# Optimization experiments

Hardware: AMD Instinct MI355X
Metric: run time of the kernel (lower is better)

Reference implementation:

```python
import jax, jax.numpy as jnp
import numpy as np
from jax import lax

B, T, I, H = 32, 512, 512, 1024


def setup_inputs() -> dict:
    key = jax.random.key(0)
    k0, k1, k2, k3, k4 = jax.random.split(key, 5)
    s_i = 1.0 / np.sqrt(I).astype(np.float32)
    s_h = 1.0 / np.sqrt(H).astype(np.float32)
    x = jax.random.normal(k0, (B, T, I), dtype=jnp.float32)
    # stacked gate weights, order: input(i), forget(f), cell(g), output(o)
    Wx = jax.random.uniform(k1, (4 * H, I), jnp.float32, -s_i, s_i)
    bx = jax.random.uniform(k2, (4 * H,), jnp.float32, -s_i, s_i)
    Wh = jax.random.uniform(k3, (4 * H, H), jnp.float32, -s_h, s_h)
    bh = jax.random.uniform(k4, (4 * H,), jnp.float32, -s_h, s_h)
    return {"x": x, "Wx": Wx, "bx": bx, "Wh": Wh, "bh": bh}


def reference(x, Wx, bx, Wh, bh):
    # Pre-compute all input-to-gate projections in one batched GEMM: [B,T,4H]
    xg = jnp.einsum("bti,gi->btg", x, Wx) + bx + bh

    def step(carry, xg_t):
        h, c = carry
        gates = xg_t + h @ Wh.T  # [B,4H]
        i, f, g, o = jnp.split(gates, 4, axis=-1)
        i = jax.nn.sigmoid(i)
        f = jax.nn.sigmoid(f)
        g = jnp.tanh(g)
        o = jax.nn.sigmoid(o)
        c = f * c + i * g
        h = o * jnp.tanh(c)  # r is None in forward -> h_tilde = tanh(c)
        return (h, c), h

    b = x.shape[0]
    h0 = jnp.zeros((b, H), dtype=x.dtype)
    c0 = jnp.zeros((b, H), dtype=x.dtype)
    _, hs = lax.scan(step, (h0, c0), jnp.swapaxes(xg, 0, 1))  # hs: [T,B,H]
    return jnp.swapaxes(hs, 0, 1)  # [B,T,H]
```

## Files before the change

kernel.cpp:

```cpp
#include <hip/hip_runtime.h>
#include <hip/hip_bf16.h>

#define Bv 32
#define Tv 512
#define Iv 512
#define Hv 1024
#define NG 4096

typedef short bf16x8 __attribute__((ext_vector_type(8)));
typedef float floatx16 __attribute__((ext_vector_type(16)));
typedef unsigned short u16;
typedef unsigned long long u64;

__device__ __forceinline__ u16 f2bf(float f) {
  __hip_bfloat16 h = __float2bfloat16(f);
  return *reinterpret_cast<u16*>(&h);
}

__device__ __forceinline__ floatx16 mfma32(bf16x8 a, bf16x8 b, floatx16 c) {
  return __builtin_amdgcn_mfma_f32_32x32x16_bf16(a, b, c, 0, 0, 0);
}

__device__ __forceinline__ u64 ld_agent_u64(const u64* p) {
  return __hip_atomic_load(p, __ATOMIC_RELAXED, __HIP_MEMORY_SCOPE_AGENT);
}
__device__ __forceinline__ void st_agent_u16(u16* p, u16 v) {
  __hip_atomic_store(p, v, __ATOMIC_RELAXED, __HIP_MEMORY_SCOPE_AGENT);
}

__device__ __forceinline__ bf16x8 mk_frag(u64 lo, u64 hi) {
  union { u64 q[2]; bf16x8 v; } u;
  u.q[0] = lo; u.q[1] = hi;
  return u.v;
}

__global__ void k_init(unsigned int* p, int n) {
  int i = blockIdx.x * blockDim.x + threadIdx.x;
  if (i < n) p[i] = 0u;
}

__global__ void k_f2bf(const float* __restrict__ in, u16* __restrict__ out, int n) {
  int i = blockIdx.x * blockDim.x + threadIdx.x;
  if (i < n) out[i] = f2bf(in[i]);
}

__global__ void k_whf(const float* __restrict__ Wh, u16* __restrict__ whf) {
  int tid = blockIdx.x * 256 + threadIdx.x;
  int lane = tid & 63;
  int kt   = (tid >> 6) & 63;
  int nt   = (tid >> 12) & 1;
  int bl   = tid >> 13;
  int r    = nt * 32 + (lane & 31);
  int gate = r >> 4, du = r & 15;
  int row  = gate * Hv + bl * 16 + du;
  int k0   = kt * 16 + (lane >> 5) * 8;
  const float* s = Wh + (size_t)row * Hv + k0;
  u16* d = whf + (size_t)tid * 8;
#pragma unroll
  for (int j = 0; j < 8; ++j) d[j] = f2bf(s[j]);
}

__global__ __launch_bounds__(256) void k_xg(const u16* __restrict__ xb, const u16* __restrict__ wxb,
                                            const float* __restrict__ bx, const float* __restrict__ bh,
                                            float* __restrict__ xg, int t0, int tcshift) {
  __shared__ u16 Al[128 * 40];
  __shared__ u16 Bl[128 * 40];
  int tid = threadIdx.x;
  int wave = tid >> 6, lane = tid & 63;
  int wm = wave & 1, wn = wave >> 1;
  int bm = blockIdx.x, bn = blockIdx.y;
  int Tc = 1 << tcshift;

  floatx16 acc[2][2];
#pragma unroll
  for (int a = 0; a < 2; ++a)
#pragma unroll
    for (int c = 0; c < 2; ++c)
#pragma unroll
      for (int r = 0; r < 16; ++r) acc[a][c][r] = 0.f;

  int lr = tid >> 1;
  int lk = (tid & 1) * 16;
  int m  = bm * 128 + lr;
  int b  = m >> tcshift;
  int tl = m & (Tc - 1);
  const u16* asrc = xb + (size_t)(b * Tv + t0 + tl) * Iv + lk;
  int nrow = bn * 128 + lr;
  const u16* bsrc = wxb + (size_t)nrow * Iv + lk;
  u16* adst = &Al[lr * 40 + lk];
  u16* bdst = &Bl[lr * 40 + lk];

  for (int k0 = 0; k0 < Iv; k0 += 32) {
    __syncthreads();
    *(uint4*)adst       = *(const uint4*)(asrc);
    *(uint4*)(adst + 8) = *(const uint4*)(asrc + 8);
    *(uint4*)bdst       = *(const uint4*)(bsrc);
    *(uint4*)(bdst + 8) = *(const uint4*)(bsrc + 8);
    asrc += 32; bsrc += 32;
    __syncthreads();
#pragma unroll
    for (int kt = 0; kt < 2; ++kt) {
      int ko = kt * 16 + (lane >> 5) * 8;
      bf16x8 a0 = *(const bf16x8*)(&Al[(wm * 64 +      (lane & 31)) * 40 + ko]);
      bf16x8 a1 = *(const bf16x8*)(&Al[(wm * 64 + 32 + (lane & 31)) * 40 + ko]);
      bf16x8 b0 = *(const bf16x8*)(&Bl[(wn * 64 +      (lane & 31)) * 40 + ko]);
      bf16x8 b1 = *(const bf16x8*)(&Bl[(wn * 64 + 32 + (lane & 31)) * 40 + ko]);
      acc[0][0] = mfma32(a0, b0, acc[0][0]);
      acc[0][1] = mfma32(a0, b1, acc[0][1]);
      acc[1][0] = mfma32(a1, b0, acc[1][0]);
      acc[1][1] = mfma32(a1, b1, acc[1][1]);
    }
  }
#pragma unroll
  for (int mt = 0; mt < 2; ++mt) {
#pragma unroll
    for (int ntt = 0; ntt < 2; ++ntt) {
      int nGl = bn * 128 + wn * 64 + ntt * 32 + (lane & 31);
      float bias = bx[nGl] + bh[nGl];
#pragma unroll
      for (int r = 0; r < 16; ++r) {
        int mrow = (r & 3) + 8 * (r >> 2) + 4 * (lane >> 5);
        int mG = bm * 128 + wm * 64 + mt * 32 + mrow;
        int bb = mG >> tcshift;
        int tt = mG & (Tc - 1);
        xg[((size_t)(tt * Bv + bb) << 12) + nGl] = acc[mt][ntt][r] + bias;
      }
    }
  }
}

__global__ __launch_bounds__(256, 1) void k_scan(const u16* __restrict__ whf, const float* __restrict__ xg,
                                                 u64* __restrict__ hA, float* __restrict__ cbuf,
                                                 float* __restrict__ out, int* cnt, int t0, int Tc) {
  __shared__ float red[4][64][36];
  int tid = threadIdx.x;
  int bl = blockIdx.x;
  int kh = tid >> 6, lane = tid & 63;
  int eu = tid & 15, eb = tid >> 4;
  int u0 = bl * 16;

  bf16x8 w0[16], w1[16];
  {
    const u16* wb0 = whf + ((size_t)(bl * 2 + 0) << 15);
    const u16* wb1 = whf + ((size_t)(bl * 2 + 1) << 15);
#pragma unroll
    for (int kk = 0; kk < 16; ++kk) {
      int kt = kh * 16 + kk;
      w0[kk] = *(const bf16x8*)(wb0 + (size_t)((kt << 6) + lane) * 8);
      w1[kk] = *(const bf16x8*)(wb1 + (size_t)((kt << 6) + lane) * 8);
    }
  }

  float c0, c1;
  if (t0 == 0) { c0 = 0.f; c1 = 0.f; }
  else {
    c0 = cbuf[eb * Hv + u0 + eu];
    c1 = cbuf[(eb + 16) * Hv + u0 + eu];
  }

  u16* hA16 = (u16*)hA;

  float xgv[4][2];
#pragma unroll
  for (int g = 0; g < 4; ++g)
#pragma unroll
    for (int b2 = 0; b2 < 2; ++b2)
      xgv[g][b2] = xg[((size_t)(0 * Bv + eb + 16 * b2) << 12) + g * Hv + u0 + eu];

  for (int tl = 0; tl < Tc; ++tl) {
    int t = t0 + tl;
    const u64* hAr = hA + (size_t)(t & 1) * 8192;

    floatx16 acc0, acc1;
#pragma unroll
    for (int r = 0; r < 16; ++r) { acc0[r] = 0.f; acc1[r] = 0.f; }
#pragma unroll
    for (int kk = 0; kk < 16; ++kk) {
      int kt = kh * 16 + kk;
      size_t fi = (size_t)((kt << 6) + lane) * 2;
      bf16x8 a = mk_frag(ld_agent_u64(hAr + fi), ld_agent_u64(hAr + fi + 1));
      acc0 = mfma32(a, w0[kk], acc0);
      acc1 = mfma32(a, w1[kk], acc1);
    }

    {
      int n = lane & 31;
      int bq = 4 * (lane >> 5);
#pragma unroll
      for (int rq = 0; rq < 4; ++rq) {
        float4 v0 = make_float4(acc0[rq * 4 + 0], acc0[rq * 4 + 1], acc0[rq * 4 + 2], acc0[rq * 4 + 3]);
        float4 v1 = make_float4(acc1[rq * 4 + 0], acc1[rq * 4 + 1], acc1[rq * 4 + 2], acc1[rq * 4 + 3]);
        *(float4*)&red[kh][n][8 * rq + bq]      = v0;
        *(float4*)&red[kh][32 + n][8 * rq + bq] = v1;
      }
    }

    float xgn[4][2];
    {
      int tln = (tl + 1 < Tc) ? tl + 1 : tl;
#pragma unroll
      for (int g = 0; g < 4; ++g)
#pragma unroll
        for (int b2 = 0; b2 < 2; ++b2)
          xgn[g][b2] = xg[((size_t)(tln * Bv + eb + 16 * b2) << 12) + g * Hv + u0 + eu];
    }

    __syncthreads();

    u16* hAw16 = hA16 + (size_t)((t + 1) & 1) * 32768;
#pragma unroll
    for (int b2 = 0; b2 < 2; ++b2) {
      int b = eb + 16 * b2;
      float gsum[4];
#pragma unroll
      for (int g = 0; g < 4; ++g) {
        int r = g * 16 + eu;
        gsum[g] = red[0][r][b] + red[1][r][b] + red[2][r][b] + red[3][r][b] + xgv[g][b2];
      }
      float iv = 1.f / (1.f + __expf(-gsum[0]));
      float fv = 1.f / (1.f + __expf(-gsum[1]));
      float gv = 1.f - 2.f / (__expf(2.f * gsum[2]) + 1.f);
      float ov = 1.f / (1.f + __expf(-gsum[3]));
      float& c = b2 ? c1 : c0;
      c = fv * c + iv * gv;
      float hval = ov * (1.f - 2.f / (__expf(2.f * c) + 1.f));
      st_agent_u16(hAw16 + ((size_t)((bl << 6) + b + ((eu >> 3) << 5)) << 3) + (eu & 7), f2bf(hval));
      out[((size_t)(b * Tv + t) << 10) + u0 + eu] = hval;
    }

    asm volatile("s_waitcnt vmcnt(0)" ::: "memory");
    __syncthreads();
    if (tid == 0) {
      __hip_atomic_fetch_add(cnt, 1, __ATOMIC_RELAXED, __HIP_MEMORY_SCOPE_AGENT);
      int target = 64 * (t + 1);
      while (__hip_atomic_load(cnt, __ATOMIC_RELAXED, __HIP_MEMORY_SCOPE_AGENT) < target) { }
    }
    __syncthreads();

#pragma unroll
    for (int g = 0; g < 4; ++g)
#pragma unroll
      for (int b2 = 0; b2 < 2; ++b2) xgv[g][b2] = xgn[g][b2];
  }
  cbuf[eb * Hv + u0 + eu] = c0;
  cbuf[(eb + 16) * Hv + u0 + eu] = c1;
}

extern "C" void kernel_launch(void* const* d_in, const int* in_sizes, int n_in,
                              void* d_out, int out_size, void* d_ws, size_t ws_size,
                              hipStream_t stream) {
  const float* x  = (const float*)d_in[0];
  const float* Wx = (const float*)d_in[1];
  const float* bx = (const float*)d_in[2];
  const float* Wh = (const float*)d_in[3];
  const float* bh = (const float*)d_in[4];
  float* out = (float*)d_out;
  char* ws = (char*)d_ws;

  int*   cnt = (int*)ws;
  u64*   hA  = (u64*)(ws + 4096);
  float* cb  = (float*)(ws + 4096 + (128 << 10));
  u16*   xb  = (u16*)(ws + 4096 + (256 << 10));
  u16*   wxb = xb + (size_t)Bv * Tv * Iv;
  u16*   whf = wxb + (size_t)NG * Iv;
  float* xg  = (float*)(whf + (size_t)64 * 2 * 64 * 64 * 8);

  size_t fixedB = 4096 + (256ull << 10) +
                  ((size_t)Bv * Tv * Iv + (size_t)NG * Iv + (size_t)64 * 2 * 64 * 64 * 8) * 2;
  int tcshift = 9;
  while (tcshift > 2 && fixedB + (((size_t)Bv * NG * 4) << tcshift) > ws_size) --tcshift;
  int Tc = 1 << tcshift;

  k_init<<<132, 256, 0, stream>>>((unsigned int*)ws, (4096 + (128 << 10)) / 4);
  k_f2bf<<<(Bv * Tv * Iv) / 256, 256, 0, stream>>>(x, xb, Bv * Tv * Iv);
  k_f2bf<<<(NG * Iv) / 256, 256, 0, stream>>>(Wx, wxb, NG * Iv);
  k_whf<<<2048, 256, 0, stream>>>(Wh, whf);

  for (int t0 = 0; t0 < Tv; t0 += Tc) {
    k_xg<<<dim3(Tc / 4, 32), 256, 0, stream>>>(xb, wxb, bx, bh, xg, t0, tcshift);
    k_scan<<<64, 256, 0, stream>>>(whf, xg, hA, cb, out, cnt, t0, Tc);
  }
}
```

Baseline: 2.675 ms.

## Replace atomic counter barrier with per-block flags and batch h loads

Replaces the single contended atomic-add counter grid barrier with per-block step flags: each block stores its step number and one wavefront polls all 64 flags, combining them with a wave vote. All h-fragment loads are now issued up front, before the MFMA chain, so their latency overlaps, and the Wh fragments are pinned in AGPRs with asm constraints. The reduction scratch is padded to 33 columns and written with scalar stores instead of float4. The aim is lower per-step barrier and load latency in the sequential scan, at the cost of more polling traffic and registers.

```diff
diff --git a/kernel.cpp b/kernel.cpp
--- a/kernel.cpp
+++ b/kernel.cpp
@@ -131,8 +131,8 @@
 
 __global__ __launch_bounds__(256, 1) void k_scan(const u16* __restrict__ whf, const float* __restrict__ xg,
                                                  u64* __restrict__ hA, float* __restrict__ cbuf,
-                                                 float* __restrict__ out, int* cnt, int t0, int Tc) {
-  __shared__ float red[4][64][36];
+                                                 float* __restrict__ out, int* flg, int t0, int Tc) {
+  __shared__ float red[4][64][33];
   int tid = threadIdx.x;
   int bl = blockIdx.x;
   int kh = tid >> 6, lane = tid & 63;
@@ -148,6 +148,8 @@
       int kt = kh * 16 + kk;
       w0[kk] = *(const bf16x8*)(wb0 + (size_t)((kt << 6) + lane) * 8);
       w1[kk] = *(const bf16x8*)(wb1 + (size_t)((kt << 6) + lane) * 8);
+      asm("" : "+a"(w0[kk]));
+      asm("" : "+a"(w1[kk]));
     }
   }
 
@@ -171,30 +173,13 @@
     int t = t0 + tl;
     const u64* hAr = hA + (size_t)(t & 1) * 8192;
 
-    floatx16 acc0, acc1;
-#pragma unroll
-    for (int r = 0; r < 16; ++r) { acc0[r] = 0.f; acc1[r] = 0.f; }
+    u64 alo[16], ahi[16];
 #pragma unroll
     for (int kk = 0; kk < 16; ++kk) {
-      int kt = kh * 16 + kk;
-      size_t fi = (size_t)((kt << 6) + lane) * 2;
-      bf16x8 a = mk_frag(ld_agent_u64(hAr + fi), ld_agent_u64(hAr + fi + 1));
-      acc0 = mfma32(a, w0[kk], acc0);
-      acc1 = mfma32(a, w1[kk], acc1);
-    }
-
-    {
-      int n = lane & 31;
-      int bq = 4 * (lane >> 5);
-#pragma unroll
-      for (int rq = 0; rq < 4; ++rq) {
-        float4 v0 = make_float4(acc0[rq * 4 + 0], acc0[rq * 4 + 1], acc0[rq * 4 + 2], acc0[rq * 4 + 3]);
-        float4 v1 = make_float4(acc1[rq * 4 + 0], acc1[rq * 4 + 1], acc1[rq * 4 + 2], acc1[rq * 4 + 3]);
-        *(float4*)&red[kh][n][8 * rq + bq]      = v0;
-        *(float4*)&red[kh][32 + n][8 * rq + bq] = v1;
-      }
-    }
-
+      size_t fi = (size_t)(((kh * 16 + kk) << 6) + lane) * 2;
+      alo[kk] = ld_agent_u64(hAr + fi);
+      ahi[kk] = ld_agent_u64(hAr + fi + 1);
+    }
     float xgn[4][2];
     {
       int tln = (tl + 1 < Tc) ? tl + 1 : tl;
@@ -205,6 +190,26 @@
           xgn[g][b2] = xg[((size_t)(tln * Bv + eb + 16 * b2) << 12) + g * Hv + u0 + eu];
     }
 
+    floatx16 acc0, acc1;
+#pragma unroll
+    for (int r = 0; r < 16; ++r) { acc0[r] = 0.f; acc1[r] = 0.f; }
+#pragma unroll
+    for (int kk = 0; kk < 16; ++kk) {
+      bf16x8 a = mk_frag(alo[kk], ahi[kk]);
+      acc0 = mfma32(a, w0[kk], acc0);
+      acc1 = mfma32(a, w1[kk], acc1);
+    }
+
+    {
+      int n = lane & 31;
+      int hoff = 4 * (lane >> 5);
+#pragma unroll
+      for (int r = 0; r < 16; ++r) {
+        int b = (r & 3) + 8 * (r >> 2) + hoff;
+        red[kh][n][b]      = acc0[r];
+        red[kh][32 + n][b] = acc1[r];
+      }
+    }
     __syncthreads();
 
     u16* hAw16 = hA16 + (size_t)((t + 1) & 1) * 32768;
@@ -230,10 +235,14 @@
 
     asm volatile("s_waitcnt vmcnt(0)" ::: "memory");
     __syncthreads();
-    if (tid == 0) {
-      __hip_atomic_fetch_add(cnt, 1, __ATOMIC_RELAXED, __HIP_MEMORY_SCOPE_AGENT);
-      int target = 64 * (t + 1);
-      while (__hip_atomic_load(cnt, __ATOMIC_RELAXED, __HIP_MEMORY_SCOPE_AGENT) < target) { }
+    if (tid == 0)
+      __hip_atomic_store(flg + bl, t + 1, __ATOMIC_RELAXED, __HIP_MEMORY_SCOPE_AGENT);
+    if (kh == 0) {
+      int target = t + 1;
+      int v;
+      do {
+        v = __hip_atomic_load(flg + lane, __ATOMIC_RELAXED, __HIP_MEMORY_SCOPE_AGENT);
+      } while (!__all(v >= target));
     }
     __syncthreads();
 
@@ -257,7 +266,7 @@
   float* out = (float*)d_out;
   char* ws = (char*)d_ws;
 
-  int*   cnt = (int*)ws;
+  int*   flg = (int*)ws;
   u64*   hA  = (u64*)(ws + 4096);
   float* cb  = (float*)(ws + 4096 + (128 << 10));
   u16*   xb  = (u16*)(ws + 4096 + (256 << 10));
@@ -278,6 +287,6 @@
 
   for (int t0 = 0; t0 < Tv; t0 += Tc) {
     k_xg<<<dim3(Tc / 4, 32), 256, 0, stream>>>(xb, wxb, bx, bh, xg, t0, tcshift);
-    k_scan<<<64, 256, 0, stream>>>(whf, xg, hA, cb, out, cnt, t0, Tc);
-  }
-}
+    k_scan<<<64, 256, 0, stream>>>(whf, xg, hA, cb, out, flg, t0, Tc);
+  }
+}
```

Result: slower. 3.331 ms (+24.5%).
